# Optimization experiments

Hardware: AMD Instinct MI355X
Metric: run time of the kernel (lower is better)

The kernel has to match this reference:

```python
import jax, jax.numpy as jnp
import numpy as np

N = 50000
E = 500000
IN_C = 100
HID = 80
OUT = 80
EDGE_DIM = 100
NUM_AGGR = 6
NUM_SCALE = 5

# PNA degree statistics, computed from the degree histogram exactly as PyG does
DEG_HIST = np.array([240, 328, 79, 39, 23, 12, 11, 7, 6, 5, 7, 3, 1, 0, 2, 0, 0, 0, 1], dtype=np.float64)
_bins = np.arange(len(DEG_HIST), dtype=np.float64)
_tot = DEG_HIST.sum()
AVG_LIN = np.float32((_bins * DEG_HIST).sum() / _tot)
AVG_LOG = np.float32((np.log(_bins + 1.0) * DEG_HIST).sum() / _tot)


def _lin_init(key, fan_in, fan_out):
    k1, k2 = jax.random.split(key)
    bound = 1.0 / np.sqrt(fan_in)
    W = jax.random.uniform(k1, (fan_in, fan_out), minval=-bound, maxval=bound, dtype=jnp.float32)
    b = jax.random.uniform(k2, (fan_out,), minval=-bound, maxval=bound, dtype=jnp.float32)
    return W, b


def setup_inputs() -> dict:
    key = jax.random.key(0)
    ks = jax.random.split(key, 20)
    inp = {}
    inp["x1"] = jax.random.normal(ks[0], (N, IN_C), jnp.float32)
    inp["edge_index1"] = jax.random.randint(ks[1], (2, E), 0, N)
    inp["edge_attr1"] = jax.random.normal(ks[2], (E, EDGE_DIM), jnp.float32)
    inp["x2"] = jax.random.normal(ks[3], (N, IN_C), jnp.float32)
    inp["edge_index2"] = jax.random.randint(ks[4], (2, E), 0, N)
    inp["edge_attr2"] = jax.random.normal(ks[5], (E, EDGE_DIM), jnp.float32)
    # conv1 params (F_in=100 -> F_out=80)
    inp["We1"], inp["be1"] = _lin_init(ks[6], EDGE_DIM, IN_C)
    inp["Wpre1"], inp["bpre1"] = _lin_init(ks[7], 3 * IN_C, IN_C)
    inp["Wpost1"], inp["bpost1"] = _lin_init(ks[8], (NUM_AGGR * NUM_SCALE + 1) * IN_C, HID)
    inp["Wlin1"], inp["blin1"] = _lin_init(ks[9], HID, HID)
    # conv2 params (F_in=80 -> F_out=80)
    inp["We2"], inp["be2"] = _lin_init(ks[10], EDGE_DIM, HID)
    inp["Wpre2"], inp["bpre2"] = _lin_init(ks[11], 3 * HID, HID)
    inp["Wpost2"], inp["bpost2"] = _lin_init(ks[12], (NUM_AGGR * NUM_SCALE + 1) * HID, OUT)
    inp["Wlin2"], inp["blin2"] = _lin_init(ks[13], OUT, OUT)
    # MLP head
    inp["Wfc1"], inp["bfc1"] = _lin_init(ks[14], OUT, 80)
    inp["Wfc2"], inp["bfc2"] = _lin_init(ks[15], 80, OUT)
    return inp


def _pna(x, src, dst, edge_attr, We, be, Wpre, bpre, Wpost, bpost, Wlin, blin):
    """PNAConv, towers=1, pre_layers=1, post_layers=1, divide_input=False."""
    F_in = x.shape[1]
    e = edge_attr @ We + be                                    # [E, F] edge encoder
    # pre_nn(cat([x_i, x_j, e])) done as 3 matmuls to avoid [E, 3F] concat
    W_i, W_j, W_e = Wpre[:F_in], Wpre[F_in:2 * F_in], Wpre[2 * F_in:]
    h = x[dst] @ W_i + x[src] @ W_j + e @ W_e + bpre           # [E, F] messages
    cnt = jax.ops.segment_sum(jnp.ones((h.shape[0],), h.dtype), dst, N)  # in-degree
    deg = jnp.maximum(cnt, 1.0)
    s = jax.ops.segment_sum(h, dst, N)                         # sum aggr
    mean = s / deg[:, None]
    mean_sq = jax.ops.segment_sum(h * h, dst, N) / deg[:, None]
    var = mean_sq - mean * mean
    std = jnp.sqrt(jnp.maximum(var, 0.0) + 1e-5)
    has = (cnt > 0)[:, None]
    mn = jnp.where(has, jax.ops.segment_min(h, dst, N), 0.0)
    mx = jnp.where(has, jax.ops.segment_max(h, dst, N), 0.0)
    agg = jnp.concatenate([s, mean, mn, mx, var, std], axis=-1)  # [N, 6F]
    logd = jnp.log(deg + 1.0)
    scaled = jnp.concatenate([
        agg,
        agg * (logd / AVG_LOG)[:, None],     # amplification
        agg * (AVG_LOG / logd)[:, None],     # attenuation
        agg * (deg / AVG_LIN)[:, None],      # linear
        agg * (AVG_LIN / deg)[:, None],      # inverse_linear
    ], axis=-1)                              # [N, 30F]
    out = jnp.concatenate([x, scaled], axis=-1) @ Wpost + bpost  # post_nn
    return out @ Wlin + blin


def _branch(x, edge_index, edge_attr, c1, c2, Wfc1, bfc1, Wfc2, bfc2):
    src, dst = edge_index[0], edge_index[1]
    x = jax.nn.relu(_pna(x, src, dst, edge_attr, *c1))
    x = _pna(x, src, dst, edge_attr, *c2)
    x = jax.nn.relu(x @ Wfc1 + bfc1)
    return x @ Wfc2 + bfc2


def reference(x1, edge_index1, edge_attr1, x2, edge_index2, edge_attr2,
              We1, be1, Wpre1, bpre1, Wpost1, bpost1, Wlin1, blin1,
              We2, be2, Wpre2, bpre2, Wpost2, bpost2, Wlin2, blin2,
              Wfc1, bfc1, Wfc2, bfc2):
    c1 = (We1, be1, Wpre1, bpre1, Wpost1, bpost1, Wlin1, blin1)
    c2 = (We2, be2, Wpre2, bpre2, Wpost2, bpost2, Wlin2, blin2)
    out1 = _branch(x1, edge_index1, edge_attr1, c1, c2, Wfc1, bfc1, Wfc2, bfc2)
    out2 = _branch(x2, edge_index2, edge_attr2, c1, c2, Wfc1, bfc1, Wfc2, bfc2)
    return (out1, out2)
```

## Files before the change

### kernel.cpp

```cpp
#include <hip/hip_runtime.h>
#include <cmath>

static constexpr int NN = 50000;
static constexpr int EE = 500000;

typedef short v8s __attribute__((ext_vector_type(8)));
typedef float v4f __attribute__((ext_vector_type(4)));

__device__ inline short f2bf(float x){
  union{float f; unsigned u;} v{x};
  unsigned r = v.u + 0x7fffu + ((v.u >> 16) & 1u);
  return (short)(r >> 16);
}
__device__ inline float b2f(short s){
  union{unsigned u; float f;} v; v.u = ((unsigned)(unsigned short)s) << 16; return v.f;
}
__device__ inline unsigned cvtpk(float lo, float hi){
  unsigned r;
  asm("v_cvt_pk_bf16_f32 %0, %1, %2" : "=v"(r) : "v"(lo), "v"(hi));
  return r;
}


__global__ __launch_bounds__(256)
void count_deg_k(const int* __restrict__ dst, int* __restrict__ cnt, int e_total){
  int e = blockIdx.x*256 + threadIdx.x;
  if (e < e_total) atomicAdd(&cnt[dst[e]], 1);
}

__global__ __launch_bounds__(1024)
void scan_block_k(const int* __restrict__ cnt, int* __restrict__ pre,
                  int* __restrict__ bsum, int n){
  __shared__ int tmp[1024];
  int b = blockIdx.x, t = threadIdx.x, i = b*1024 + t;
  int v = (i < n) ? cnt[i] : 0;
  tmp[t] = v; __syncthreads();
  for (int off = 1; off < 1024; off <<= 1){
    int u = (t >= off) ? tmp[t-off] : 0;
    __syncthreads();
    tmp[t] += u;
    __syncthreads();
  }
  if (i < n) pre[i] = tmp[t];
  if (t == 1023) bsum[b] = tmp[t];
}

__global__ void scan_sums_k(int* __restrict__ bsum, int nb){
  if (threadIdx.x == 0){
    int s = 0;
    for (int i = 0; i < nb; i++){ int v = bsum[i]; bsum[i] = s; s += v; }
  }
}

__global__ __launch_bounds__(256)
void scan_finalize_k(const int* __restrict__ pre, const int* __restrict__ bsum,
                     int* __restrict__ offs, int n){
  int i = blockIdx.x*256 + threadIdx.x;
  if (i < n) offs[i+1] = pre[i] + bsum[i >> 10];
  if (i == 0) offs[0] = 0;
}

__global__ __launch_bounds__(256)
void fill_csr_k(const int* __restrict__ dst, const int* __restrict__ src,
                const int* __restrict__ offs, int* __restrict__ cursor,
                int2* __restrict__ edg, int e_total){
  int e = blockIdx.x*256 + threadIdx.x;
  if (e < e_total){
    int d = dst[e];
    int p = offs[d] + atomicAdd(&cursor[d], 1);
    edg[p] = make_int2(e, src[e]);
  }
}


struct VJob { const float* v; const float* B; const float* b2; float* out; int K, Nc; };
struct VJobs { VJob j[3]; };
__global__ __launch_bounds__(128)
void vecmat_multi_k(VJobs js){
  const VJob J = js.j[blockIdx.y];
  int c = threadIdx.x;
  if (c < J.Nc){
    float s = J.b2[c];
    for (int k = 0; k < J.K; k++) s += J.v[k]*J.B[(size_t)k*J.Nc + c];
    J.out[c] = s;
  }
}

__global__ __launch_bounds__(256)
void sgemm_k(const float* __restrict__ A, const float* __restrict__ B,
             float* __restrict__ C, int M, int K, int Nc){
  __shared__ float As[16][65];
  __shared__ float Bs[16][65];
  int bm = blockIdx.x*64, bn = blockIdx.y*64;
  int tid = threadIdx.x;
  int tx = tid & 15, ty = tid >> 4;
  float acc[4][4] = {};
  for (int k0 = 0; k0 < K; k0 += 16){
    #pragma unroll
    for (int i = 0; i < 4; i++){
      int t = tid + 256*i;
      int r = t >> 4, c = t & 15;
      int gr = bm + r, gc = k0 + c;
      As[c][r] = (gr < M && gc < K) ? A[(size_t)gr*K + gc] : 0.f;
    }
    #pragma unroll
    for (int i = 0; i < 4; i++){
      int t = tid + 256*i;
      int r = t >> 6, c = t & 63;
      int gr = k0 + r, gc = bn + c;
      Bs[r][c] = (gr < K && gc < Nc) ? B[(size_t)gr*Nc + gc] : 0.f;
    }
    __syncthreads();
    #pragma unroll
    for (int kk = 0; kk < 16; kk++){
      float a[4], b[4];
      #pragma unroll
      for (int i = 0; i < 4; i++) a[i] = As[kk][ty*4 + i];
      #pragma unroll
      for (int j = 0; j < 4; j++) b[j] = Bs[kk][tx*4 + j];
      #pragma unroll
      for (int i = 0; i < 4; i++)
        #pragma unroll
        for (int j = 0; j < 4; j++) acc[i][j] += a[i]*b[j];
    }
    __syncthreads();
  }
  #pragma unroll
  for (int i = 0; i < 4; i++){
    int gr = bm + ty*4 + i;
    if (gr >= M) continue;
    #pragma unroll
    for (int j = 0; j < 4; j++){
      int gc = bn + tx*4 + j;
      if (gc < Nc) C[(size_t)gr*Nc + gc] = acc[i][j];
    }
  }
}

struct TJob { const float* src; short* dst; int K, ldsrc, Ncols; };
struct TJobs { TJob j[9]; };
__global__ __launch_bounds__(128)
void tconv_multi_k(TJobs js){
  const TJob J = js.j[blockIdx.y];
  int c = blockIdx.x;
  int k = threadIdx.x;
  if (c < J.Ncols)
    J.dst[(long)c*128 + k] = (k < J.K) ? f2bf(J.src[(long)k*J.ldsrc + c]) : (short)0;
}

__global__ __launch_bounds__(256)
void btpost_k(const float* __restrict__ Wpost, int F, int Kpad,
              short* __restrict__ dst){
  int cp = blockIdx.x;
  int k = blockIdx.y*256 + threadIdx.x;
  if (k >= Kpad) return;
  int g = cp / 80, c = cp - g*80;
  float v = 0.f;
  if (k < F){ if (g == 0) v = Wpost[(long)k*80 + c]; }
  else if (k < 7*F) v = Wpost[(long)(F + g*6*F + (k - F))*80 + c];
  dst[(long)cp*Kpad + k] = f2bf(v);
}

__global__ __launch_bounds__(256)
void cvt_rows_k(const float* __restrict__ src, int K, short* __restrict__ dst,
                int ldd, long total){
  long i = (long)blockIdx.x*256 + threadIdx.x;
  if (i >= total) return;
  int n = (int)(i / K), c = (int)(i - (long)n*K);
  dst[(long)n*ldd + c] = f2bf(src[i]);
}

struct ZJob { short* p; int ld, c0, nc, rows; };
struct ZJobs { ZJob j[4]; };
__global__ __launch_bounds__(256)
void zeropad_k(ZJobs js){
  const ZJob J = js.j[blockIdx.y];
  int i = blockIdx.x*256 + threadIdx.x;
  int r = i / J.nc, c = i - r*J.nc;
  if (r < J.rows) J.p[(long)r*J.ld + J.c0 + c] = 0;
}

template<int NFR, bool A_F32, bool C_F32, bool RELU>
__global__ __launch_bounds__(256)
void egemm_k(const void* __restrict__ Av, long lda, int Kreal,
             const short* __restrict__ Bt, const float* __restrict__ bias,
             void* __restrict__ Cv, long ldc, int M, int ncols, int wlim)
{
  constexpr int BN = NFR*16;
  constexpr int PITCH = BN + 8;
  constexpr int NCH = 2*NFR;
  __shared__ short Bs[BN][136];
  __shared__ short stage[4*8*PITCH];
  const float* Af = (const float*)Av;
  const short* Ab = (const short*)Av;
  short* Cb = (short*)Cv;
  float* Cf = (float*)Cv;

  int bn = blockIdx.y*BN;
  for (int u = threadIdx.x; u < BN*16; u += 256){
    int c = u >> 4, k8 = (u & 15)*8;
    v8s vv = (v8s)0;
    if (bn + c < ncols) vv = *(const v8s*)(Bt + (long)(bn + c)*128 + k8);
    *(v8s*)&Bs[c][k8] = vv;
  }
  __syncthreads();

  int lane = threadIdx.x & 63;
  int lr = lane & 15, lkg = lane >> 4;
  int w = threadIdx.x >> 6;
  short* st = stage + w*8*PITCH;
  int w0 = (blockIdx.x*256 + threadIdx.x) >> 6;
  int nw = gridDim.x * 4;
  int Mtiles = (M + 31) >> 5;

  float bvs[NFR];
  #pragma unroll
  for (int n = 0; n < NFR; n++) bvs[n] = bias ? bias[bn + n*16 + lr] : 0.f;

  for (int t = w0; t < Mtiles; t += nw){
    int base = t*32;
    long r0 = base + lr;      if (r0 > M-1) r0 = M-1;
    long r1 = base + 16 + lr; if (r1 > M-1) r1 = M-1;

    v8s a0[4], a1[4];
    if constexpr (A_F32){
      const float* p0 = Af + r0*lda;
      const float* p1 = Af + r1*lda;
      float4 f0[8], f1[8];
      #pragma unroll
      for (int ks = 0; ks < 4; ks++){
        int kb = ks*32 + lkg*8;
        bool ok0 = (kb + 3 < Kreal), ok1 = (kb + 7 < Kreal);
        f0[ks*2+0] = ok0 ? *(const float4*)(p0 + kb)     : make_float4(0.f,0.f,0.f,0.f);
        f0[ks*2+1] = ok1 ? *(const float4*)(p0 + kb + 4) : make_float4(0.f,0.f,0.f,0.f);
        f1[ks*2+0] = ok0 ? *(const float4*)(p1 + kb)     : make_float4(0.f,0.f,0.f,0.f);
        f1[ks*2+1] = ok1 ? *(const float4*)(p1 + kb + 4) : make_float4(0.f,0.f,0.f,0.f);
      }
      #pragma unroll
      for (int ks = 0; ks < 4; ks++){
        union { v8s s; unsigned u[4]; } o0, o1;
        o0.u[0] = cvtpk(f0[ks*2].x, f0[ks*2].y);
        o0.u[1] = cvtpk(f0[ks*2].z, f0[ks*2].w);
        o0.u[2] = cvtpk(f0[ks*2+1].x, f0[ks*2+1].y);
        o0.u[3] = cvtpk(f0[ks*2+1].z, f0[ks*2+1].w);
        o1.u[0] = cvtpk(f1[ks*2].x, f1[ks*2].y);
        o1.u[1] = cvtpk(f1[ks*2].z, f1[ks*2].w);
        o1.u[2] = cvtpk(f1[ks*2+1].x, f1[ks*2+1].y);
        o1.u[3] = cvtpk(f1[ks*2+1].z, f1[ks*2+1].w);
        a0[ks] = o0.s; a1[ks] = o1.s;
      }
    } else {
      const short* p0 = Ab + r0*lda + lkg*8;
      const short* p1 = Ab + r1*lda + lkg*8;
      #pragma unroll
      for (int ks = 0; ks < 4; ks++){
        a0[ks] = *(const v8s*)(p0 + ks*32);
        a1[ks] = *(const v8s*)(p1 + ks*32);
      }
    }

    v4f acc0[NFR], acc1[NFR];
    #pragma unroll
    for (int n = 0; n < NFR; n++){ acc0[n] = (v4f)0.f; acc1[n] = (v4f)0.f; }
    #pragma unroll
    for (int ks = 0; ks < 4; ks++){
      #pragma unroll
      for (int n = 0; n < NFR; n++){
        v8s b = *(const v8s*)&Bs[n*16 + lr][ks*32 + lkg*8];
        acc0[n] = __builtin_amdgcn_mfma_f32_16x16x32_bf16(a0[ks], b, acc0[n], 0, 0, 0);
        acc1[n] = __builtin_amdgcn_mfma_f32_16x16x32_bf16(a1[ks], b, acc1[n], 0, 0, 0);
      }
    }

    if constexpr (C_F32){
      #pragma unroll
      for (int n = 0; n < NFR; n++){
        int col = bn + n*16 + lr;
        if (col >= ncols) continue;
        #pragma unroll
        for (int j = 0; j < 4; j++){
          int row = base + lkg*4 + j;
          float v0 = acc0[n][j] + bvs[n];
          float v1 = acc1[n][j] + bvs[n];
          if (RELU){ v0 = fmaxf(v0, 0.f); v1 = fmaxf(v1, 0.f); }
          if (row < M)      Cf[(long)row*ldc + col] = v0;
          if (row + 16 < M) Cf[(long)(row+16)*ldc + col] = v1;
        }
      }
    } else {
      #pragma unroll
      for (int q = 0; q < 4; q++){
        if ((lkg >> 1) == (q & 1)){
          int srow = (lkg & 1)*4;
          #pragma unroll
          for (int n = 0; n < NFR; n++){
            #pragma unroll
            for (int j = 0; j < 4; j++){
              float v = ((q < 2) ? acc0[n][j] : acc1[n][j]) + bvs[n];
              if (RELU) v = fmaxf(v, 0.f);
              st[(srow + j)*PITCH + n*16 + lr] = f2bf(v);
            }
          }
        }
        int rb = base + q*8;
        #pragma unroll
        for (int i = 0; i < (8*NCH + 63)/64; i++){
          int c = i*64 + lane;
          if (c < 8*NCH){
            int r = c/NCH, off8 = (c - r*NCH)*8;
            int grow = rb + r;
            if (grow < M && bn + off8 < wlim)
              *(v8s*)(Cb + (long)grow*ldc + bn + off8) = *(const v8s*)&st[r*PITCH + off8];
          }
        }
      }
    }
  }
}

__global__ __launch_bounds__(512)
void pgemm_k(const short* __restrict__ Ab, int kpad,
             const short* __restrict__ Bt, const float* __restrict__ scl,
             const float* __restrict__ bias, short* __restrict__ C, int M)
{
  __shared__ short Bs[400][40];
  __shared__ short AsSt[10240];
  short (*As)[40] = (short(*)[40])AsSt;

  int tid = threadIdx.x;
  int w = tid >> 6, lane = tid & 63;
  int lr = lane & 15, lkg = lane >> 4;
  int bm = blockIdx.x*128;

  v4f acc[25];
  #pragma unroll
  for (int n = 0; n < 25; n++) acc[n] = (v4f)0.f;

  for (int k0 = 0; k0 < kpad; k0 += 32){
    {
      int u = tid;
      int r = u >> 2, c8 = (u & 3)*8;
      int grow = bm + r;
      v8s out = (v8s)0;
      if (grow < M) out = *(const v8s*)(Ab + (long)grow*kpad + k0 + c8);
      *(v8s*)&As[r][c8] = out;
    }
    for (int u = tid; u < 400*4; u += 512){
      int c = u >> 2, k8 = (u & 3)*8;
      *(v8s*)&Bs[c][k8] = *(const v8s*)(Bt + (long)c*kpad + k0 + k8);
    }
    __syncthreads();
    {
      v8s a = *(const v8s*)&As[w*16 + lr][lkg*8];
      #pragma unroll
      for (int n = 0; n < 25; n++){
        v8s b = *(const v8s*)&Bs[n*16 + lr][lkg*8];
        acc[n] = __builtin_amdgcn_mfma_f32_16x16x32_bf16(a, b, acc[n], 0, 0, 0);
      }
    }
    __syncthreads();
  }

  short* st = AsSt + w*16*80;
  float sc[4][5];
  #pragma unroll
  for (int j = 0; j < 4; j++){
    int row = bm + w*16 + lkg*4 + j;
    int rr = row < M ? row : 0;
    #pragma unroll
    for (int g = 0; g < 5; g++) sc[j][g] = scl[rr*5 + g];
  }
  #pragma unroll
  for (int cc = 0; cc < 5; cc++){
    float bv = bias[cc*16 + lr];
    #pragma unroll
    for (int j = 0; j < 4; j++){
      float v = bv;
      #pragma unroll
      for (int g = 0; g < 5; g++) v += sc[j][g]*acc[5*g + cc][j];
      st[(lkg*4 + j)*80 + cc*16 + lr] = f2bf(v);
    }
  }
  #pragma unroll
  for (int i = 0; i < 3; i++){
    int c = i*64 + lane;
    if (c < 160){
      int r = c/10, off = (c - r*10)*8;
      int grow = bm + w*16 + r;
      if (grow < M)
        *(v8s*)(C + (long)grow*128 + off) = *(const v8s*)&st[r*80 + off];
    }
  }
}

template<int F>
__global__ __launch_bounds__(256)
void aggregate_k(const short* __restrict__ xixj, int ldx,
                 const short* __restrict__ epc, int epoff,
                 const int2* __restrict__ edg,
                 const int* __restrict__ offs,
                 short* __restrict__ aggout, long ldk,
                 float* __restrict__ scl, float avg_lin, float avg_log, int n){
  int wnode = (blockIdx.x*256 + threadIdx.x) >> 6;
  int lane = threadIdx.x & 63;
  if (wnode >= n) return;
  constexpr int C2 = F - 64;
  int beg = offs[wnode], end = offs[wnode+1];
  float xi0 = b2f(xixj[(long)wnode*ldx + lane]);
  float xi1 = (lane < C2) ? b2f(xixj[(long)wnode*ldx + 64 + lane]) : 0.f;
  float s0 = 0.f, q0 = 0.f, mn0 = INFINITY, mx0 = -INFINITY;
  float s1 = 0.f, q1 = 0.f, mn1 = INFINITY, mx1 = -INFINITY;
  for (int p = beg; p < end; p++){
    int2 es = edg[p];
    long e = es.x; int s = es.y;
    float h0 = xi0 + b2f(xixj[(long)s*ldx + F + lane]) + b2f(epc[e*192 + epoff + lane]);
    s0 += h0; q0 += h0*h0; mn0 = fminf(mn0, h0); mx0 = fmaxf(mx0, h0);
    if (lane < C2){
      float h1 = xi1 + b2f(xixj[(long)s*ldx + F + 64 + lane]) + b2f(epc[e*192 + epoff + 64 + lane]);
      s1 += h1; q1 += h1*h1; mn1 = fminf(mn1, h1); mx1 = fmaxf(mx1, h1);
    }
  }
  int cnt = end - beg;
  float deg = (float)(cnt > 1 ? cnt : 1);
  if (cnt == 0){ mn0 = 0.f; mx0 = 0.f; mn1 = 0.f; mx1 = 0.f; }
  float mean0 = s0/deg, var0 = q0/deg - mean0*mean0;
  float std0 = sqrtf(fmaxf(var0, 0.f) + 1e-5f);
  short* a = aggout + (long)wnode*ldk;
  a[lane] = f2bf(s0); a[F+lane] = f2bf(mean0); a[2*F+lane] = f2bf(mn0);
  a[3*F+lane] = f2bf(mx0); a[4*F+lane] = f2bf(var0); a[5*F+lane] = f2bf(std0);
  if (lane < C2){
    float mean1 = s1/deg, var1 = q1/deg - mean1*mean1;
    float std1 = sqrtf(fmaxf(var1, 0.f) + 1e-5f);
    int l2 = 64 + lane;
    a[l2] = f2bf(s1); a[F+l2] = f2bf(mean1); a[2*F+l2] = f2bf(mn1);
    a[3*F+l2] = f2bf(mx1); a[4*F+l2] = f2bf(var1); a[5*F+l2] = f2bf(std1);
  }
  if (lane == 0){
    float logd = logf(deg + 1.f);
    scl[wnode*5+0] = 1.f;
    scl[wnode*5+1] = logd/avg_log;
    scl[wnode*5+2] = avg_log/logd;
    scl[wnode*5+3] = deg/avg_lin;
    scl[wnode*5+4] = avg_lin/deg;
  }
}


extern "C" void kernel_launch(void* const* d_in, const int* in_sizes, int n_in,
                              void* d_out, int out_size, void* d_ws, size_t ws_size,
                              hipStream_t stream){
  const float* x1   = (const float*)d_in[0];
  const int*   ei1  = (const int*)  d_in[1];
  const float* ea1  = (const float*)d_in[2];
  const float* x2   = (const float*)d_in[3];
  const int*   ei2  = (const int*)  d_in[4];
  const float* ea2  = (const float*)d_in[5];
  const float* We1  = (const float*)d_in[6],  *be1   = (const float*)d_in[7];
  const float* Wpre1= (const float*)d_in[8],  *bpre1 = (const float*)d_in[9];
  const float* Wpost1=(const float*)d_in[10], *bpost1= (const float*)d_in[11];
  const float* Wlin1= (const float*)d_in[12], *blin1 = (const float*)d_in[13];
  const float* We2  = (const float*)d_in[14], *be2   = (const float*)d_in[15];
  const float* Wpre2= (const float*)d_in[16], *bpre2 = (const float*)d_in[17];
  const float* Wpost2=(const float*)d_in[18], *bpost2= (const float*)d_in[19];
  const float* Wlin2= (const float*)d_in[20], *blin2 = (const float*)d_in[21];
  const float* Wfc1 = (const float*)d_in[22], *bfc1  = (const float*)d_in[23];
  const float* Wfc2 = (const float*)d_in[24], *bfc2  = (const float*)d_in[25];

  static const double HIST[19] = {240,328,79,39,23,12,11,7,6,5,7,3,1,0,2,0,0,0,1};
  double tot = 0, lin = 0, lg = 0;
  for (int i = 0; i < 19; i++){ tot += HIST[i]; lin += i*HIST[i]; lg += log((double)i + 1.0)*HIST[i]; }
  float avg_lin = (float)(lin/tot), avg_log = (float)(lg/tot);

  const int KP1 = 704, KP2 = 576;

  uintptr_t pw = (uintptr_t)d_ws;
  auto carve = [&](size_t b)->void*{ void* r = (void*)pw; pw += (b + 255) & ~(size_t)255; return r; };
  int*   cnt      = (int*)  carve((size_t)NN*4);
  int*   cursor   = (int*)  carve((size_t)NN*4);
  int*   pre      = (int*)  carve((size_t)NN*4);
  int*   bsum     = (int*)  carve(64*4);
  int*   offs     = (int*)  carve((size_t)(NN+1)*4);
  int2*  edg      = (int2*) carve((size_t)EE*8);
  float* WecA     = (float*)carve(100*100*4);
  float* WecB     = (float*)carve(100*80*4);
  float* Wlf      = (float*)carve(80*80*4);
  float* becf     = (float*)carve(256*4);
  float* blf      = (float*)carve(128*4);
  short* Btep12   = (short*)carve((size_t)192*128*2);
  short* Btij1    = (short*)carve((size_t)208*128*2);
  short* Btij2    = (short*)carve((size_t)160*128*2);
  short* Btpost1  = (short*)carve((size_t)400*KP1*2);
  short* Btpost2  = (short*)carve((size_t)400*KP2*2);
  short* Btlin1   = (short*)carve((size_t)80*128*2);
  short* Btlf     = (short*)carve((size_t)80*128*2);
  short* Btfc2    = (short*)carve((size_t)80*128*2);
  short* Aprime1  = (short*)carve((size_t)NN*KP1*2);
  short* Aprime2  = (short*)carve((size_t)NN*KP2*2);
  short* xixjb    = (short*)carve((size_t)NN*224*2);
  short* epc      = (short*)carve((size_t)EE*192*2);
  float* scl      = (float*)carve((size_t)NN*5*4);
  short* tpost    = (short*)carve((size_t)NN*128*2);
  short* tD       = (short*)carve((size_t)NN*128*2);

  dim3 blk(256);
  const int NB = (NN + 1023)/1024;
  const int GB_N = 391;
  const int GB_E = 1024;

  sgemm_k<<<dim3(2,2), blk, 0, stream>>>(We1, Wpre1 + 2*100*100, WecA, 100, 100, 100);
  sgemm_k<<<dim3(2,2), blk, 0, stream>>>(We2, Wpre2 + 2*80*80,  WecB, 100, 80, 80);
  sgemm_k<<<dim3(2,2), blk, 0, stream>>>(Wlin2, Wfc1, Wlf, 80, 80, 80);
  hipMemsetAsync(becf, 0, 256*4, stream);
  {
    VJobs vj;
    vj.j[0] = {be1,  Wpre1 + 2*100*100, bpre1, becf,       100, 100};
    vj.j[1] = {be2,  Wpre2 + 2*80*80,   bpre2, becf + 100,  80,  80};
    vj.j[2] = {blin2, Wfc1,             bfc1,  blf,         80,  80};
    vecmat_multi_k<<<dim3(1,3), dim3(128), 0, stream>>>(vj);
  }
  {
    TJobs tj;
    tj.j[0] = {WecA,            Btep12,            100, 100, 100};
    tj.j[1] = {WecB,            Btep12 + 100*128,  100,  80,  80};
    tj.j[2] = {Wpre1,           Btij1,             100, 100, 100};
    tj.j[3] = {Wpre1 + 100*100, Btij1 + 100*128,   100, 100, 100};
    tj.j[4] = {Wpre2,           Btij2,              80,  80,  80};
    tj.j[5] = {Wpre2 + 80*80,   Btij2 + 80*128,     80,  80,  80};
    tj.j[6] = {Wlin1,           Btlin1,             80,  80,  80};
    tj.j[7] = {Wlf,             Btlf,               80,  80,  80};
    tj.j[8] = {Wfc2,            Btfc2,              80,  80,  80};
    tconv_multi_k<<<dim3(100,9), dim3(128), 0, stream>>>(tj);
  }
  btpost_k<<<dim3(400,(KP1+255)/256), blk, 0, stream>>>(Wpost1, 100, KP1, Btpost1);
  btpost_k<<<dim3(400,(KP2+255)/256), blk, 0, stream>>>(Wpost2,  80, KP2, Btpost2);
  {
    ZJobs zj;
    zj.j[0] = {Aprime1, KP1, 700,  4, NN};
    zj.j[1] = {Aprime2, KP2, 560, 16, NN};
    zj.j[2] = {tpost,   128,  80, 48, NN};
    zj.j[3] = {tD,      128,  80, 48, NN};
    zeropad_k<<<dim3((NN*48 + 255)/256, 4), blk, 0, stream>>>(zj);
  }

  for (int b = 0; b < 2; b++){
    const float* x  = b ? x2  : x1;
    const int*   ei = b ? ei2 : ei1;
    const float* ea = b ? ea2 : ea1;
    float* outb = (float*)d_out + (size_t)b*NN*80;
    const int* src = ei;
    const int* dst = ei + EE;

    hipMemsetAsync(cnt, 0, (uintptr_t)pre - (uintptr_t)cnt, stream);
    count_deg_k<<<dim3((EE+255)/256), blk, 0, stream>>>(dst, cnt, EE);
    scan_block_k<<<dim3(NB), dim3(1024), 0, stream>>>(cnt, pre, bsum, NN);
    scan_sums_k<<<dim3(1), dim3(64), 0, stream>>>(bsum, NB);
    scan_finalize_k<<<dim3((NN+255)/256), blk, 0, stream>>>(pre, bsum, offs, NN);
    fill_csr_k<<<dim3((EE+255)/256), blk, 0, stream>>>(dst, src, offs, cursor, edg, EE);

    egemm_k<6,true,false,false><<<dim3(GB_E,2), blk, 0, stream>>>(
        ea, 100, 100, Btep12, becf, epc, 192, EE, 180, 192);

    cvt_rows_k<<<dim3((int)(((long)NN*100 + 255)/256)), blk, 0, stream>>>(x, 100, Aprime1, KP1, (long)NN*100);

    egemm_k<5,false,false,false><<<dim3(GB_N,3), blk, 0, stream>>>(
        Aprime1, KP1, 0, Btij1, nullptr, xixjb, 224, NN, 200, 200);
    aggregate_k<100><<<dim3((NN+3)/4), blk, 0, stream>>>(
        xixjb, 224, epc, 0, edg, offs, Aprime1 + 100, KP1, scl, avg_lin, avg_log, NN);
    pgemm_k<<<dim3((NN+127)/128), dim3(512), 0, stream>>>(
        Aprime1, KP1, Btpost1, scl, bpost1, tpost, NN);
    egemm_k<5,false,false,true><<<dim3(GB_N,1), blk, 0, stream>>>(
        tpost, 128, 0, Btlin1, blin1, Aprime2, KP2, NN, 80, 80);

    egemm_k<5,false,false,false><<<dim3(GB_N,2), blk, 0, stream>>>(
        Aprime2, KP2, 0, Btij2, nullptr, xixjb, 160, NN, 160, 160);
    aggregate_k<80><<<dim3((NN+3)/4), blk, 0, stream>>>(
        xixjb, 160, epc, 100, edg, offs, Aprime2 + 80, KP2, scl, avg_lin, avg_log, NN);
    pgemm_k<<<dim3((NN+127)/128), dim3(512), 0, stream>>>(
        Aprime2, KP2, Btpost2, scl, bpost2, tpost, NN);

    egemm_k<5,false,false,true><<<dim3(GB_N,1), blk, 0, stream>>>(
        tpost, 128, 0, Btlf, blf, tD, 128, NN, 80, 80);
    egemm_k<5,false,true,false><<<dim3(GB_N,1), blk, 0, stream>>>(
        tD, 128, 0, Btfc2, bfc2, outb, 80, NN, 80, 80);
  }
}
```

Baseline: 1.322 ms.

## Write edge projections in CSR order via dedicated LDS-staged edge GEMM

Adds a dedicated edge-projection GEMM that streams edge_attr rows into LDS with global_load_lds and keeps the B fragments in registers. It scatters each projected row to its CSR position, so epc is stored in destination-sorted order. The aggregation kernels then read epc contiguously by CSR index p and only need a plain int source array, replacing the random per-edge gathers through the (e,src) pairs. In exchange the GEMM's output writes become scattered 384-byte rows, and the kernel depends on zero-padded B rows, which new memsets provide.

```diff
diff --git a/kernel.cpp b/kernel.cpp
--- a/kernel.cpp
+++ b/kernel.cpp
@@ -19,6 +19,12 @@
   unsigned r;
   asm("v_cvt_pk_bf16_f32 %0, %1, %2" : "=v"(r) : "v"(lo), "v"(hi));
   return r;
+}
+__device__ inline void gload16(const void* gp, void* lp){
+  __builtin_amdgcn_global_load_lds(
+      (const __attribute__((address_space(1))) void*)gp,
+      (__attribute__((address_space(3))) void*)lp,
+      16, 0, 0);
 }
 
 
@@ -63,12 +69,13 @@
 __global__ __launch_bounds__(256)
 void fill_csr_k(const int* __restrict__ dst, const int* __restrict__ src,
                 const int* __restrict__ offs, int* __restrict__ cursor,
-                int2* __restrict__ edg, int e_total){
+                int* __restrict__ srcs_csr, int* __restrict__ pos, int e_total){
   int e = blockIdx.x*256 + threadIdx.x;
   if (e < e_total){
     int d = dst[e];
     int p = offs[d] + atomicAdd(&cursor[d], 1);
-    edg[p] = make_int2(e, src[e]);
+    srcs_csr[p] = src[e];
+    pos[e] = p;
   }
 }
 
@@ -180,9 +187,101 @@
   if (r < J.rows) J.p[(long)r*J.ld + J.c0 + c] = 0;
 }
 
-template<int NFR, bool A_F32, bool C_F32, bool RELU>
-__global__ __launch_bounds__(256)
-void egemm_k(const void* __restrict__ Av, long lda, int Kreal,
+__global__ __launch_bounds__(256)
+void epgemm_k(const float* __restrict__ ea,
+              const short* __restrict__ Bt,
+              const float* __restrict__ bias,
+              const int* __restrict__ pos,
+              short* __restrict__ epc)
+{
+  __shared__ float Atile[3456];
+  __shared__ short stage[32*200];
+  int tid = threadIdx.x, w = tid >> 6, lane = tid & 63;
+  int lr = lane & 15, lkg = lane >> 4;
+
+  v8s bfrag[3][4];
+  float bvs[3];
+  #pragma unroll
+  for (int n = 0; n < 3; n++){
+    int col = w*48 + n*16 + lr;
+    bvs[n] = bias[col];
+    #pragma unroll
+    for (int ks = 0; ks < 4; ks++)
+      bfrag[n][ks] = *(const v8s*)(Bt + (long)col*128 + ks*32 + lkg*8);
+  }
+
+  const char* srcbase = (const char*)ea;
+  const char* srcend  = srcbase + (long)EE*400 - 16;
+  const int Mtiles = EE/32;
+
+  for (int t = blockIdx.x; t < Mtiles; t += gridDim.x){
+    long tb = (long)t*12800;
+    for (int c = w; c < 13; c += 4){
+      const char* src = srcbase + tb + (long)c*1024 + lane*16;
+      if (src > srcend) src = srcend;
+      gload16(src, (char*)Atile + c*1024);
+    }
+    __syncthreads();
+
+    const float* rp0 = Atile + lr*100;
+    const float* rp1 = Atile + (16 + lr)*100;
+    v8s a0[4], a1[4];
+    #pragma unroll
+    for (int ks = 0; ks < 4; ks++){
+      float4 lo0, hi0, lo1, hi1;
+      if (ks < 3){
+        int kb = ks*32 + lkg*8;
+        lo0 = *(const float4*)(rp0 + kb); hi0 = *(const float4*)(rp0 + kb + 4);
+        lo1 = *(const float4*)(rp1 + kb); hi1 = *(const float4*)(rp1 + kb + 4);
+      } else {
+        float4 z = make_float4(0.f,0.f,0.f,0.f);
+        lo0 = (lkg == 0) ? *(const float4*)(rp0 + 96) : z;
+        lo1 = (lkg == 0) ? *(const float4*)(rp1 + 96) : z;
+        hi0 = z; hi1 = z;
+      }
+      union { v8s s; unsigned u[4]; } o0, o1;
+      o0.u[0] = cvtpk(lo0.x, lo0.y); o0.u[1] = cvtpk(lo0.z, lo0.w);
+      o0.u[2] = cvtpk(hi0.x, hi0.y); o0.u[3] = cvtpk(hi0.z, hi0.w);
+      o1.u[0] = cvtpk(lo1.x, lo1.y); o1.u[1] = cvtpk(lo1.z, lo1.w);
+      o1.u[2] = cvtpk(hi1.x, hi1.y); o1.u[3] = cvtpk(hi1.z, hi1.w);
+      a0[ks] = o0.s; a1[ks] = o1.s;
+    }
+    v4f acc0[3], acc1[3];
+    #pragma unroll
+    for (int n = 0; n < 3; n++){ acc0[n] = (v4f)0.f; acc1[n] = (v4f)0.f; }
+    #pragma unroll
+    for (int ks = 0; ks < 4; ks++){
+      #pragma unroll
+      for (int n = 0; n < 3; n++){
+        acc0[n] = __builtin_amdgcn_mfma_f32_16x16x32_bf16(a0[ks], bfrag[n][ks], acc0[n], 0, 0, 0);
+        acc1[n] = __builtin_amdgcn_mfma_f32_16x16x32_bf16(a1[ks], bfrag[n][ks], acc1[n], 0, 0, 0);
+      }
+    }
+
+    #pragma unroll
+    for (int n = 0; n < 3; n++){
+      int col = w*48 + n*16 + lr;
+      #pragma unroll
+      for (int j = 0; j < 4; j++){
+        stage[(lkg*4 + j)*200 + col]      = f2bf(acc0[n][j] + bvs[n]);
+        stage[(16 + lkg*4 + j)*200 + col] = f2bf(acc1[n][j] + bvs[n]);
+      }
+    }
+    __syncthreads();
+
+    #pragma unroll
+    for (int i = 0; i < 3; i++){
+      int u = i*256 + tid;
+      int r = u / 24, ch = u - r*24;
+      int prow = pos[t*32 + r];
+      *(v8s*)(epc + (long)prow*192 + ch*8) = *(const v8s*)&stage[r*200 + ch*8];
+    }
+  }
+}
+
+template<int NFR, bool C_F32, bool RELU>
+__global__ __launch_bounds__(256)
+void egemm_k(const short* __restrict__ Ab, long lda,
              const short* __restrict__ Bt, const float* __restrict__ bias,
              void* __restrict__ Cv, long ldc, int M, int ncols, int wlim)
 {
@@ -191,8 +290,6 @@
   constexpr int NCH = 2*NFR;
   __shared__ short Bs[BN][136];
   __shared__ short stage[4*8*PITCH];
-  const float* Af = (const float*)Av;
-  const short* Ab = (const short*)Av;
   short* Cb = (short*)Cv;
   float* Cf = (float*)Cv;
 
@@ -223,40 +320,12 @@
     long r1 = base + 16 + lr; if (r1 > M-1) r1 = M-1;
 
     v8s a0[4], a1[4];
-    if constexpr (A_F32){
-      const float* p0 = Af + r0*lda;
-      const float* p1 = Af + r1*lda;
-      float4 f0[8], f1[8];
-      #pragma unroll
-      for (int ks = 0; ks < 4; ks++){
-        int kb = ks*32 + lkg*8;
-        bool ok0 = (kb + 3 < Kreal), ok1 = (kb + 7 < Kreal);
-        f0[ks*2+0] = ok0 ? *(const float4*)(p0 + kb)     : make_float4(0.f,0.f,0.f,0.f);
-        f0[ks*2+1] = ok1 ? *(const float4*)(p0 + kb + 4) : make_float4(0.f,0.f,0.f,0.f);
-        f1[ks*2+0] = ok0 ? *(const float4*)(p1 + kb)     : make_float4(0.f,0.f,0.f,0.f);
-        f1[ks*2+1] = ok1 ? *(const float4*)(p1 + kb + 4) : make_float4(0.f,0.f,0.f,0.f);
-      }
-      #pragma unroll
-      for (int ks = 0; ks < 4; ks++){
-        union { v8s s; unsigned u[4]; } o0, o1;
-        o0.u[0] = cvtpk(f0[ks*2].x, f0[ks*2].y);
-        o0.u[1] = cvtpk(f0[ks*2].z, f0[ks*2].w);
-        o0.u[2] = cvtpk(f0[ks*2+1].x, f0[ks*2+1].y);
-        o0.u[3] = cvtpk(f0[ks*2+1].z, f0[ks*2+1].w);
-        o1.u[0] = cvtpk(f1[ks*2].x, f1[ks*2].y);
-        o1.u[1] = cvtpk(f1[ks*2].z, f1[ks*2].w);
-        o1.u[2] = cvtpk(f1[ks*2+1].x, f1[ks*2+1].y);
-        o1.u[3] = cvtpk(f1[ks*2+1].z, f1[ks*2+1].w);
-        a0[ks] = o0.s; a1[ks] = o1.s;
-      }
-    } else {
-      const short* p0 = Ab + r0*lda + lkg*8;
-      const short* p1 = Ab + r1*lda + lkg*8;
-      #pragma unroll
-      for (int ks = 0; ks < 4; ks++){
-        a0[ks] = *(const v8s*)(p0 + ks*32);
-        a1[ks] = *(const v8s*)(p1 + ks*32);
-      }
+    const short* p0 = Ab + r0*lda + lkg*8;
+    const short* p1 = Ab + r1*lda + lkg*8;
+    #pragma unroll
+    for (int ks = 0; ks < 4; ks++){
+      a0[ks] = *(const v8s*)(p0 + ks*32);
+      a1[ks] = *(const v8s*)(p1 + ks*32);
     }
 
     v4f acc0[NFR], acc1[NFR];
@@ -397,7 +466,7 @@
 __global__ __launch_bounds__(256)
 void aggregate_k(const short* __restrict__ xixj, int ldx,
                  const short* __restrict__ epc, int epoff,
-                 const int2* __restrict__ edg,
+                 const int* __restrict__ srcs_csr,
                  const int* __restrict__ offs,
                  short* __restrict__ aggout, long ldk,
                  float* __restrict__ scl, float avg_lin, float avg_log, int n){
@@ -411,12 +480,11 @@
   float s0 = 0.f, q0 = 0.f, mn0 = INFINITY, mx0 = -INFINITY;
   float s1 = 0.f, q1 = 0.f, mn1 = INFINITY, mx1 = -INFINITY;
   for (int p = beg; p < end; p++){
-    int2 es = edg[p];
-    long e = es.x; int s = es.y;
-    float h0 = xi0 + b2f(xixj[(long)s*ldx + F + lane]) + b2f(epc[e*192 + epoff + lane]);
+    int s = srcs_csr[p];
+    float h0 = xi0 + b2f(xixj[(long)s*ldx + F + lane]) + b2f(epc[(long)p*192 + epoff + lane]);
     s0 += h0; q0 += h0*h0; mn0 = fminf(mn0, h0); mx0 = fmaxf(mx0, h0);
     if (lane < C2){
-      float h1 = xi1 + b2f(xixj[(long)s*ldx + F + 64 + lane]) + b2f(epc[e*192 + epoff + 64 + lane]);
+      float h1 = xi1 + b2f(xixj[(long)s*ldx + F + 64 + lane]) + b2f(epc[(long)p*192 + epoff + 64 + lane]);
       s1 += h1; q1 += h1*h1; mn1 = fminf(mn1, h1); mx1 = fmaxf(mx1, h1);
     }
   }
@@ -480,7 +548,8 @@
   int*   pre      = (int*)  carve((size_t)NN*4);
   int*   bsum     = (int*)  carve(64*4);
   int*   offs     = (int*)  carve((size_t)(NN+1)*4);
-  int2*  edg      = (int2*) carve((size_t)EE*8);
+  int*   srcs_csr = (int*)  carve((size_t)EE*4);
+  int*   pos      = (int*)  carve((size_t)EE*4);
   float* WecA     = (float*)carve(100*100*4);
   float* WecB     = (float*)carve(100*80*4);
   float* Wlf      = (float*)carve(80*80*4);
@@ -505,7 +574,6 @@
   dim3 blk(256);
   const int NB = (NN + 1023)/1024;
   const int GB_N = 391;
-  const int GB_E = 1024;
 
   sgemm_k<<<dim3(2,2), blk, 0, stream>>>(We1, Wpre1 + 2*100*100, WecA, 100, 100, 100);
   sgemm_k<<<dim3(2,2), blk, 0, stream>>>(We2, Wpre2 + 2*80*80,  WecB, 100, 80, 80);
@@ -531,6 +599,8 @@
     tj.j[8] = {Wfc2,            Btfc2,              80,  80,  80};
     tconv_multi_k<<<dim3(100,9), dim3(128), 0, stream>>>(tj);
   }
+  hipMemsetAsync(Btep12 + 180*128, 0, (size_t)12*128*2, stream);
+  hipMemsetAsync(Btij1 + 200*128, 0, (size_t)8*128*2, stream);
   btpost_k<<<dim3(400,(KP1+255)/256), blk, 0, stream>>>(Wpost1, 100, KP1, Btpost1);
   btpost_k<<<dim3(400,(KP2+255)/256), blk, 0, stream>>>(Wpost2,  80, KP2, Btpost2);
   {
@@ -555,32 +625,31 @@
     scan_block_k<<<dim3(NB), dim3(1024), 0, stream>>>(cnt, pre, bsum, NN);
     scan_sums_k<<<dim3(1), dim3(64), 0, stream>>>(bsum, NB);
     scan_finalize_k<<<dim3((NN+255)/256), blk, 0, stream>>>(pre, bsum, offs, NN);
-    fill_csr_k<<<dim3((EE+255)/256), blk, 0, stream>>>(dst, src, offs, cursor, edg, EE);
-
-    egemm_k<6,true,false,false><<<dim3(GB_E,2), blk, 0, stream>>>(
-        ea, 100, 100, Btep12, becf, epc, 192, EE, 180, 192);
+    fill_csr_k<<<dim3((EE+255)/256), blk, 0, stream>>>(dst, src, offs, cursor, srcs_csr, pos, EE);
+
+    epgemm_k<<<dim3(2048), blk, 0, stream>>>(ea, Btep12, becf, pos, epc);
 
     cvt_rows_k<<<dim3((int)(((long)NN*100 + 255)/256)), blk, 0, stream>>>(x, 100, Aprime1, KP1, (long)NN*100);
 
-    egemm_k<5,false,false,false><<<dim3(GB_N,3), blk, 0, stream>>>(
-        Aprime1, KP1, 0, Btij1, nullptr, xixjb, 224, NN, 200, 200);
+    egemm_k<5,false,false><<<dim3(GB_N,3), blk, 0, stream>>>(
+        Aprime1, KP1, Btij1, nullptr, xixjb, 224, NN, 200, 200);
     aggregate_k<100><<<dim3((NN+3)/4), blk, 0, stream>>>(
-        xixjb, 224, epc, 0, edg, offs, Aprime1 + 100, KP1, scl, avg_lin, avg_log, NN);
+        xixjb, 224, epc, 0, srcs_csr, offs, Aprime1 + 100, KP1, scl, avg_lin, avg_log, NN);
     pgemm_k<<<dim3((NN+127)/128), dim3(512), 0, stream>>>(
         Aprime1, KP1, Btpost1, scl, bpost1, tpost, NN);
-    egemm_k<5,false,false,true><<<dim3(GB_N,1), blk, 0, stream>>>(
-        tpost, 128, 0, Btlin1, blin1, Aprime2, KP2, NN, 80, 80);
-
-    egemm_k<5,false,false,false><<<dim3(GB_N,2), blk, 0, stream>>>(
-        Aprime2, KP2, 0, Btij2, nullptr, xixjb, 160, NN, 160, 160);
+    egemm_k<5,false,true><<<dim3(GB_N,1), blk, 0, stream>>>(
+        tpost, 128, Btlin1, blin1, Aprime2, KP2, NN, 80, 80);
+
+    egemm_k<5,false,false><<<dim3(GB_N,2), blk, 0, stream>>>(
+        Aprime2, KP2, Btij2, nullptr, xixjb, 160, NN, 160, 160);
     aggregate_k<80><<<dim3((NN+3)/4), blk, 0, stream>>>(
-        xixjb, 160, epc, 100, edg, offs, Aprime2 + 80, KP2, scl, avg_lin, avg_log, NN);
+        xixjb, 160, epc, 100, srcs_csr, offs, Aprime2 + 80, KP2, scl, avg_lin, avg_log, NN);
     pgemm_k<<<dim3((NN+127)/128), dim3(512), 0, stream>>>(
         Aprime2, KP2, Btpost2, scl, bpost2, tpost, NN);
 
-    egemm_k<5,false,false,true><<<dim3(GB_N,1), blk, 0, stream>>>(
-        tpost, 128, 0, Btlf, blf, tD, 128, NN, 80, 80);
-    egemm_k<5,false,true,false><<<dim3(GB_N,1), blk, 0, stream>>>(
-        tD, 128, 0, Btfc2, bfc2, outb, 80, NN, 80, 80);
-  }
-}
+    egemm_k<5,false,true><<<dim3(GB_N,1), blk, 0, stream>>>(
+        tpost, 128, Btlf, blf, tD, 128, NN, 80, 80);
+    egemm_k<5,true,false><<<dim3(GB_N,1), blk, 0, stream>>>(
+        tD, 128, Btfc2, bfc2, outb, 80, NN, 80, 80);
+  }
+}
```

New measurement: 1.222 ms. 1.08x faster.
